# Kernel tuning notes

Measured on AMD Instinct MI355X. Metric: run time of the kernel, lower is better.

## Reference

```python
import jax, jax.numpy as jnp
import numpy as np


def setup_inputs() -> dict:
    key = jax.random.key(0)
    k1, k2 = jax.random.split(key)
    B, N, M, C = 32, 4096, 4096, 3
    xyz1 = jax.random.normal(k1, (B, N, C), dtype=jnp.float32)
    xyz2 = jax.random.normal(k2, (B, M, C), dtype=jnp.float32)
    return {"xyz1": xyz1, "xyz2": xyz2}


def _chamfer_l2(xyz1, xyz2):
    # Pairwise squared L2 distances via ||a||^2 + ||b||^2 - 2 a.b  (b n m)
    sq1 = jnp.sum(xyz1 * xyz1, axis=-1)            # [B, N]
    sq2 = jnp.sum(xyz2 * xyz2, axis=-1)            # [B, M]
    cross = jnp.einsum('bnc,bmc->bnm', xyz1, xyz2) # [B, N, M]
    d = sq1[:, :, None] + sq2[:, None, :] - 2.0 * cross
    dist1 = jnp.min(d, axis=2)                     # [B, N] nearest in xyz2
    dist2 = jnp.min(d, axis=1)                     # [B, M] nearest in xyz1
    return jnp.mean(dist1, axis=-1) + jnp.mean(dist2, axis=-1)  # [B]


def reference(xyz1, xyz2):
    return _chamfer_l2(xyz1, xyz2)
```

## Files before the change

kernel.cpp:

```cpp
#include <hip/hip_runtime.h>

typedef _Float16 half8 __attribute__((ext_vector_type(8)));
typedef float floatx16 __attribute__((ext_vector_type(16)));

#define TPB   256
#define RPTS  1024
#define NTILE (RPTS / 32)
#define SMH   (RPTS * 16)

__global__ __launch_bounds__(TPB, 4) void chamfer_mfma(const float* __restrict__ xyz1,
                                                       const float* __restrict__ xyz2,
                                                       float* __restrict__ out,
                                                       int N, int M) {
    const int b = blockIdx.y, dir = blockIdx.z;
    const float* __restrict__ P = dir ? xyz2 + (size_t)b * M * 3 : xyz1 + (size_t)b * N * 3;
    const float* __restrict__ Q = dir ? xyz1 + (size_t)b * N * 3 : xyz2 + (size_t)b * M * 3;
    const int nq = dir ? M : N;
    const int md = dir ? N : M;

    if ((int)blockIdx.x * TPB >= nq) return;

    __shared__ __align__(16) _Float16 smB[SMH];

    const int tid = (int)threadIdx.x;
    const int w   = tid >> 6;
    const int l   = tid & 63;
    const int m   = l & 31;
    const int h   = l >> 5;

    const _Float16 hz = (_Float16)0.0f, hone = (_Float16)1.0f;
    const int qb = blockIdx.x * 256 + w * 64;

    half8 afr[2];
#pragma unroll
    for (int g = 0; g < 2; ++g) {
        int idx = qb + g * 32 + m;
        int ci  = idx < nq ? idx : nq - 1;
        float x = P[3 * ci], y = P[3 * ci + 1], z = P[3 * ci + 2];
        _Float16 xh = (_Float16)x, yh = (_Float16)y, zh = (_Float16)z;
        _Float16 xl = (_Float16)(x - (float)xh);
        _Float16 yl = (_Float16)(y - (float)yh);
        _Float16 zl = (_Float16)(z - (float)zh);
        half8 a;
        if (h == 0) {
            a[0] = -xh; a[1] = -xh; a[2] = -xl; a[3] = -yh;
            a[4] = -yh; a[5] = -yl; a[6] = -zh; a[7] = -zh;
        } else {
            a[0] = -zl; a[1] = hone; a[2] = hone; a[3] = hz;
            a[4] = hz;  a[5] = hz;   a[6] = hz;  a[7] = hz;
        }
        afr[g] = a;
    }

    float rm[32];
#pragma unroll
    for (int i = 0; i < 32; ++i) rm[i] = 3.0e38f;

    const floatx16 czero = {0.0f, 0.0f, 0.0f, 0.0f, 0.0f, 0.0f, 0.0f, 0.0f,
                            0.0f, 0.0f, 0.0f, 0.0f, 0.0f, 0.0f, 0.0f, 0.0f};
    const int nrounds = (md + RPTS - 1) / RPTS;
    const _Float16* bp = smB + h * 256 + m * 8;

    for (int r = 0; r < nrounds; ++r) {
        if (r) __syncthreads();
#pragma unroll
        for (int k = 0; k < RPTS / TPB; ++k) {
            int j = tid + k * TPB;
            int g = r * RPTS + j;
            g = g < md ? g : md - 1;
            float x = Q[3 * g], y = Q[3 * g + 1], z = Q[3 * g + 2];
            float hq = 0.5f * (x * x + y * y + z * z);
            _Float16 xh = (_Float16)x, yh = (_Float16)y, zh = (_Float16)z;
            _Float16 xl = (_Float16)(x - (float)xh);
            _Float16 yl = (_Float16)(y - (float)yh);
            _Float16 zl = (_Float16)(z - (float)zh);
            _Float16 qh = (_Float16)hq;
            _Float16 ql = (_Float16)(hq - (float)qh);
            int t = j >> 5, c = j & 31;
            half8 v0, v1;
            v0[0] = xh; v0[1] = xl; v0[2] = xh; v0[3] = yh;
            v0[4] = yl; v0[5] = yh; v0[6] = zh; v0[7] = zl;
            v1[0] = zh; v1[1] = qh; v1[2] = ql; v1[3] = hz;
            v1[4] = hz; v1[5] = hz; v1[6] = hz; v1[7] = hz;
            *(half8*)&smB[t * 512 + c * 8]       = v0;
            *(half8*)&smB[t * 512 + 256 + c * 8] = v1;
        }
        __syncthreads();

        for (int t = 0; t < NTILE; t += 2) {
            half8 b0 = *(const half8*)(bp + t * 512);
            half8 b1 = *(const half8*)(bp + t * 512 + 512);
            floatx16 d0a = __builtin_amdgcn_mfma_f32_32x32x16_f16(afr[0], b0, czero, 0, 0, 0);
            floatx16 d0b = __builtin_amdgcn_mfma_f32_32x32x16_f16(afr[0], b1, czero, 0, 0, 0);
#pragma unroll
            for (int i = 0; i < 16; ++i)
                rm[i] = fminf(fminf(rm[i], d0a[i]), d0b[i]);
            floatx16 d1a = __builtin_amdgcn_mfma_f32_32x32x16_f16(afr[1], b0, czero, 0, 0, 0);
            floatx16 d1b = __builtin_amdgcn_mfma_f32_32x32x16_f16(afr[1], b1, czero, 0, 0, 0);
#pragma unroll
            for (int i = 0; i < 16; ++i)
                rm[16 + i] = fminf(fminf(rm[16 + i], d1a[i]), d1b[i]);
        }
    }

#pragma unroll
    for (int off = 1; off < 32; off <<= 1) {
#pragma unroll
        for (int i = 0; i < 32; ++i) rm[i] = fminf(rm[i], __shfl_xor(rm[i], off, 64));
    }

    float s = 0.0f;
    if (m < 16) {
        const int reg = (m & 3) + 4 * (m >> 2);
        const int row = 4 * h + (m & 3) + 8 * (m >> 2);
#pragma unroll
        for (int g = 0; g < 2; ++g) {
            int idx = qb + g * 32 + row;
            if (idx < nq) {
                float x = P[3 * idx], y = P[3 * idx + 1], z = P[3 * idx + 2];
                s += rm[g * 16 + reg] + 0.5f * (x * x + y * y + z * z);
            }
        }
    }
#pragma unroll
    for (int off = 32; off > 0; off >>= 1) s += __shfl_down(s, off, 64);
    if (l == 0) atomicAdd(out + b, s * (2.0f / (float)nq));
}

extern "C" void kernel_launch(void* const* d_in, const int* in_sizes, int n_in,
                              void* d_out, int out_size, void* d_ws, size_t ws_size,
                              hipStream_t stream) {
    const float* xyz1 = (const float*)d_in[0];
    const float* xyz2 = (const float*)d_in[1];
    float* out = (float*)d_out;

    const int B = out_size;
    const int N = in_sizes[0] / (3 * B);
    const int M = in_sizes[1] / (3 * B);

    hipMemsetAsync(d_out, 0, (size_t)B * sizeof(float), stream);

    const int qmax = N > M ? N : M;
    dim3 grid((qmax + 255) / 256, B, 2);
    chamfer_mfma<<<grid, dim3(TPB), 0, stream>>>(xyz1, xyz2, out, N, M);
}
```

Measured before the change: 115.5 us.

## Double-buffer reference point tiles in LDS with register prefetch

Replaces the single 1024-point LDS tile with two 512-point buffers. Global loads for round r+2 are prefetched into registers while the tile for round r+1 is written to the alternate buffer before the MFMA loop over round r runs, so each round needs only one barrier. The aim is to hide global load latency and barrier stalls behind MFMA work. In exchange there are more rounds, extra live registers for the prefetched points, and total LDS use per block stays the same.

```diff
diff --git a/kernel.cpp b/kernel.cpp
--- a/kernel.cpp
+++ b/kernel.cpp
@@ -4,9 +4,30 @@
 typedef float floatx16 __attribute__((ext_vector_type(16)));
 
 #define TPB   256
-#define RPTS  1024
+#define RPTS  512
 #define NTILE (RPTS / 32)
 #define SMH   (RPTS * 16)
+
+
+__device__ __forceinline__ void wr_point(_Float16* __restrict__ smb, int j,
+                                         float x, float y, float z) {
+    float hq = 0.5f * (x * x + y * y + z * z);
+    _Float16 xh = (_Float16)x, yh = (_Float16)y, zh = (_Float16)z;
+    _Float16 xl = (_Float16)(x - (float)xh);
+    _Float16 yl = (_Float16)(y - (float)yh);
+    _Float16 zl = (_Float16)(z - (float)zh);
+    _Float16 qh = (_Float16)hq;
+    _Float16 ql = (_Float16)(hq - (float)qh);
+    const _Float16 hz = (_Float16)0.0f;
+    int t = j >> 5, c = j & 31;
+    half8 v0, v1;
+    v0[0] = xh; v0[1] = xl; v0[2] = xh; v0[3] = yh;
+    v0[4] = yl; v0[5] = yh; v0[6] = zh; v0[7] = zl;
+    v1[0] = zh; v1[1] = qh; v1[2] = ql; v1[3] = hz;
+    v1[4] = hz; v1[5] = hz; v1[6] = hz; v1[7] = hz;
+    *(half8*)&smb[t * 512 + c * 8]       = v0;
+    *(half8*)&smb[t * 512 + 256 + c * 8] = v1;
+}
 
 __global__ __launch_bounds__(TPB, 4) void chamfer_mfma(const float* __restrict__ xyz1,
                                                        const float* __restrict__ xyz2,
@@ -20,7 +41,7 @@
 
     if ((int)blockIdx.x * TPB >= nq) return;
 
-    __shared__ __align__(16) _Float16 smB[SMH];
+    __shared__ __align__(16) _Float16 smB[2][SMH];
 
     const int tid = (int)threadIdx.x;
     const int w   = tid >> 6;
@@ -52,6 +73,20 @@
         afr[g] = a;
     }
 
+    float sx0, sy0, sz0, sx1, sy1, sz1;
+#define LDPTS(rr) {                                                   \
+        int g0 = (rr) * RPTS + tid;                                   \
+        int g1 = g0 + TPB;                                            \
+        g0 = g0 < md ? g0 : md - 1;   \
+        g1 = g1 < md ? g1 : md - 1;                                   \
+        sx0 = Q[3 * g0]; sy0 = Q[3 * g0 + 1]; sz0 = Q[3 * g0 + 2];    \
+        sx1 = Q[3 * g1]; sy1 = Q[3 * g1 + 1]; sz1 = Q[3 * g1 + 2];    \
+    }
+#define WRPTS(bb) {                                                   \
+        wr_point(&smB[bb][0], tid,       sx0, sy0, sz0);              \
+        wr_point(&smB[bb][0], tid + TPB, sx1, sy1, sz1);              \
+    }
+
     float rm[32];
 #pragma unroll
     for (int i = 0; i < 32; ++i) rm[i] = 3.0e38f;
@@ -59,34 +94,23 @@
     const floatx16 czero = {0.0f, 0.0f, 0.0f, 0.0f, 0.0f, 0.0f, 0.0f, 0.0f,
                             0.0f, 0.0f, 0.0f, 0.0f, 0.0f, 0.0f, 0.0f, 0.0f};
     const int nrounds = (md + RPTS - 1) / RPTS;
-    const _Float16* bp = smB + h * 256 + m * 8;
 
+    LDPTS(0);
+    WRPTS(0);
+    if (nrounds > 1) LDPTS(1);
+    __syncthreads();
+
+    const _Float16* bp0 = &smB[0][h * 256 + m * 8];
+    const _Float16* bp1 = &smB[1][h * 256 + m * 8];
+
+    int cur = 0;
     for (int r = 0; r < nrounds; ++r) {
-        if (r) __syncthreads();
-#pragma unroll
-        for (int k = 0; k < RPTS / TPB; ++k) {
-            int j = tid + k * TPB;
-            int g = r * RPTS + j;
-            g = g < md ? g : md - 1;
-            float x = Q[3 * g], y = Q[3 * g + 1], z = Q[3 * g + 2];
-            float hq = 0.5f * (x * x + y * y + z * z);
-            _Float16 xh = (_Float16)x, yh = (_Float16)y, zh = (_Float16)z;
-            _Float16 xl = (_Float16)(x - (float)xh);
-            _Float16 yl = (_Float16)(y - (float)yh);
-            _Float16 zl = (_Float16)(z - (float)zh);
-            _Float16 qh = (_Float16)hq;
-            _Float16 ql = (_Float16)(hq - (float)qh);
-            int t = j >> 5, c = j & 31;
-            half8 v0, v1;
-            v0[0] = xh; v0[1] = xl; v0[2] = xh; v0[3] = yh;
-            v0[4] = yl; v0[5] = yh; v0[6] = zh; v0[7] = zl;
-            v1[0] = zh; v1[1] = qh; v1[2] = ql; v1[3] = hz;
-            v1[4] = hz; v1[5] = hz; v1[6] = hz; v1[7] = hz;
-            *(half8*)&smB[t * 512 + c * 8]       = v0;
-            *(half8*)&smB[t * 512 + 256 + c * 8] = v1;
+        if (r + 1 < nrounds) {
+            WRPTS(cur ^ 1);
+            if (r + 2 < nrounds) LDPTS(r + 2);
         }
-        __syncthreads();
 
+        const _Float16* bp = cur ? bp1 : bp0;
         for (int t = 0; t < NTILE; t += 2) {
             half8 b0 = *(const half8*)(bp + t * 512);
             half8 b1 = *(const half8*)(bp + t * 512 + 512);
@@ -101,6 +125,9 @@
             for (int i = 0; i < 16; ++i)
                 rm[16 + i] = fminf(fminf(rm[16 + i], d1a[i]), d1b[i]);
         }
+
+        if (r + 1 < nrounds) __syncthreads();
+        cur ^= 1;
     }
 
 #pragma unroll
```

New measurement: 122.4 us. 1.06x slower.
